# Optimization experiments

Hardware: AMD Instinct MI355X
Metric: run time of the kernel (lower is better)

Reference implementation:

```python
import jax, jax.numpy as jnp
import numpy as np

NODE_DIM = 128
OUT_DIM = 64
N_NODES = 50000
N_EDGES = 800000
NEG_SLOPE = 0.01  # F.leaky_relu default


def setup_inputs() -> dict:
    key = jax.random.key(0)
    k1, k2, k3, k4, k5 = jax.random.split(key, 5)
    h = jax.random.normal(k1, (N_NODES, NODE_DIM), dtype=jnp.float32)
    src = jax.random.randint(k2, (N_EDGES,), 0, N_NODES, dtype=jnp.int32)
    dst = jax.random.randint(k3, (N_EDGES,), 0, N_NODES, dtype=jnp.int32)
    # fc: Linear(node_dim, out_dim, bias=False); attn_fc: Linear(2*out_dim, 1, bias=False)
    W_fc = jax.random.normal(k4, (NODE_DIM, OUT_DIM), dtype=jnp.float32) * (1.0 / np.sqrt(NODE_DIM))
    W_attn = jax.random.normal(k5, (2 * OUT_DIM, 1), dtype=jnp.float32) * (1.0 / np.sqrt(2 * OUT_DIM))
    return {"h": h, "src": src, "dst": dst, "W_fc": W_fc, "W_attn": W_attn}


def reference(h, src, dst, W_fc, W_attn):
    N = h.shape[0]
    D = W_fc.shape[1]
    z = h @ W_fc                                   # [N, D]
    # attn_fc(concat(z_src, z_dst)) == z_src @ Wa[:D] + z_dst @ Wa[D:]
    s_src = (z @ W_attn[:D]).squeeze(-1)            # [N]
    s_dst = (z @ W_attn[D:]).squeeze(-1)            # [N]
    e = jax.nn.leaky_relu(s_src[src] + s_dst[dst], NEG_SLOPE)  # [E]
    # segment softmax over incoming edges per dst node
    m = jax.ops.segment_max(e, dst, num_segments=N)            # [N]
    ex = jnp.exp(e - m[dst])                                   # [E]
    denom = jax.ops.segment_sum(ex, dst, num_segments=N)       # [N]
    alpha = ex / denom[dst]                                    # [E]
    # weighted scatter-sum of src features into dst nodes
    out = jax.ops.segment_sum(alpha[:, None] * z[src], dst, num_segments=N)  # [N, D]
    return out
```

## Files before the change

### kernel.cpp

```cpp
#include <hip/hip_runtime.h>

#define NODE_DIM 128
#define OUT_DIM  64
#define NEG_SLOPE 0.01f
#define EPB    4096
#define BSH    7
#define NPB    128
#define REGCAP 2400

typedef __attribute__((ext_vector_type(8))) short short8;
typedef __attribute__((ext_vector_type(4))) short short4v;
typedef __attribute__((ext_vector_type(4))) float float4e;

__device__ __forceinline__ unsigned short f2bf(float f) {
    unsigned u = __float_as_uint(f);
    unsigned r = (u + 0x7FFFu + ((u >> 16) & 1u)) >> 16;
    return (unsigned short)r;
}
__device__ __forceinline__ float bf2f(unsigned short v) {
    return __uint_as_float((unsigned)v << 16);
}
__device__ __forceinline__ void split_bf(float v, short& hi, short& lo) {
    unsigned short h = f2bf(v);
    float r = v - bf2f(h);
    hi = (short)h;
    lo = (short)f2bf(r);
}

__global__ __launch_bounds__(256) void k_proj_part(
    const float* __restrict__ h, const float* __restrict__ Wf,
    const float* __restrict__ Wa,
    unsigned short* __restrict__ zbf,
    float* __restrict__ s_src, float* __restrict__ s_dst,
    const int* __restrict__ src, const int* __restrict__ dst,
    int* __restrict__ region, int* __restrict__ bcur,
    int N, int E, int nblkP, int NB)
{
    __shared__ union {
        short w[16384];
        unsigned short zt[4][16][68];
        struct { int sd[EPB]; int sv[EPB]; } p;
    } uni;
    __shared__ int cnt[512];
    __shared__ int bb[512];
    __shared__ int rr[512];
    __shared__ int ps[256];

    if (blockIdx.x < (unsigned)nblkP) {
        const int blk = blockIdx.x;
        const int t = threadIdx.x;
        cnt[t] = 0; cnt[t + 256] = 0;
        __syncthreads();
        const int e0 = blk * EPB;
        int nE = E - e0; if (nE > EPB) nE = EPB;

        int db[16], sb[16], rreg[16];
        const int base = e0 + t * 16;
        if (base + 16 <= E) {
            const int4* dp = (const int4*)(dst + base);
            const int4* sp = (const int4*)(src + base);
            #pragma unroll
            for (int q = 0; q < 4; ++q) {
                int4 dv = dp[q], svv = sp[q];
                db[q*4+0]=dv.x; db[q*4+1]=dv.y; db[q*4+2]=dv.z; db[q*4+3]=dv.w;
                sb[q*4+0]=svv.x; sb[q*4+1]=svv.y; sb[q*4+2]=svv.z; sb[q*4+3]=svv.w;
            }
            #pragma unroll
            for (int k = 0; k < 16; ++k)
                rreg[k] = atomicAdd(&cnt[db[k] >> BSH], 1);
        } else {
            #pragma unroll
            for (int k = 0; k < 16; ++k) rreg[k] = -1;
            for (int k = 0; k < 16; ++k) {
                int idx = base + k;
                if (idx < E) {
                    db[k] = dst[idx];
                    sb[k] = src[idx];
                    rreg[k] = atomicAdd(&cnt[db[k] >> BSH], 1);
                }
            }
        }
        __syncthreads();

        int pv = cnt[2 * t] + cnt[2 * t + 1];
        ps[t] = pv;
        __syncthreads();
        #pragma unroll
        for (int off = 1; off < 256; off <<= 1) {
            int u = (t >= off) ? ps[t - off] : 0;
            __syncthreads();
            ps[t] += u;
            __syncthreads();
        }
        int pexc = ps[t] - pv;
        bb[2 * t]     = pexc;
        bb[2 * t + 1] = pexc + cnt[2 * t];
        __syncthreads();

        #pragma unroll
        for (int k = 0; k < 16; ++k) {
            if (rreg[k] >= 0) {
                int pos = bb[db[k] >> BSH] + rreg[k];
                uni.p.sd[pos] = db[k];
                uni.p.sv[pos] = sb[k];
            }
        }
        for (int i = t; i < NB; i += 256) {
            int cb = cnt[i];
            rr[i] = cb ? atomicAdd(bcur + i, cb) : 0;
        }
        __syncthreads();

        for (int j = t; j < nE; j += 256) {
            int d = uni.p.sd[j];
            int b = d >> BSH;
            int gp = rr[b] + (j - bb[b]);
            if (gp < REGCAP)
                region[(size_t)b * REGCAP + gp] = ((d & (NPB - 1)) << 17) | uni.p.sv[j];
        }
        return;
    }

    const int bid  = blockIdx.x - nblkP;
    const int t    = threadIdx.x;
    const int wv   = t >> 6;
    const int lane = t & 63;
    const int m    = lane & 15;
    const int quad = lane >> 4;
    const int row0 = bid * 64 + wv * 16;

    int rowc = row0 + m; if (rowc > N - 1) rowc = N - 1;
    const float* hrow = h + (size_t)rowc * NODE_DIM;
    float4e hreg[8];
    #pragma unroll
    for (int t4 = 0; t4 < 4; ++t4) {
        hreg[t4 * 2]     = *(const float4e*)(hrow + t4 * 32 + quad * 8);
        hreg[t4 * 2 + 1] = *(const float4e*)(hrow + t4 * 32 + quad * 8 + 4);
    }

    {
        short* wh = uni.w;
        short* wl = uni.w + 8192;
        for (int s = t; s < 1024; s += 256) {
            int combo = s >> 6;
            int ln    = s & 63;
            int c = combo >> 2, t4 = combo & 3;
            int col = c * 16 + (ln & 15);
            int kq  = t4 * 32 + (ln >> 4) * 8;
            #pragma unroll
            for (int j = 0; j < 8; ++j) {
                short hi, lo;
                split_bf(Wf[(kq + j) * OUT_DIM + col], hi, lo);
                wh[s * 8 + j] = hi;
                wl[s * 8 + j] = lo;
            }
        }
    }
    __syncthreads();

    short8 Ahi[4], Alo[4];
    #pragma unroll
    for (int t4 = 0; t4 < 4; ++t4) {
        #pragma unroll
        for (int j = 0; j < 4; ++j) {
            short hi, lo;
            split_bf(hreg[t4 * 2][j], hi, lo);
            Ahi[t4][j] = hi; Alo[t4][j] = lo;
            split_bf(hreg[t4 * 2 + 1][j], hi, lo);
            Ahi[t4][4 + j] = hi; Alo[t4][4 + j] = lo;
        }
    }

    float psum[4] = {0.f, 0.f, 0.f, 0.f};
    float pdum[4] = {0.f, 0.f, 0.f, 0.f};
    unsigned short z16[16];

    const short* wh = uni.w;
    const short* wl = uni.w + 8192;
    #pragma unroll
    for (int c = 0; c < 4; ++c) {
        float4e acc = {0.f, 0.f, 0.f, 0.f};
        #pragma unroll
        for (int t4 = 0; t4 < 4; ++t4) {
            int slot = (c * 4 + t4) * 64 + lane;
            short8 bh = *(const short8*)(wh + slot * 8);
            short8 bl = *(const short8*)(wl + slot * 8);
            acc = __builtin_amdgcn_mfma_f32_16x16x32_bf16(Alo[t4], bh, acc, 0, 0, 0);
            acc = __builtin_amdgcn_mfma_f32_16x16x32_bf16(Ahi[t4], bl, acc, 0, 0, 0);
            acc = __builtin_amdgcn_mfma_f32_16x16x32_bf16(Ahi[t4], bh, acc, 0, 0, 0);
        }
        int col = c * 16 + m;
        float was = Wa[col];
        float wad = Wa[OUT_DIM + col];
        #pragma unroll
        for (int r = 0; r < 4; ++r) {
            z16[c * 4 + r] = f2bf(acc[r]);
            psum[r] = fmaf(acc[r], was, psum[r]);
            pdum[r] = fmaf(acc[r], wad, pdum[r]);
        }
    }

    #pragma unroll
    for (int r = 0; r < 4; ++r) {
        #pragma unroll
        for (int off = 1; off < 16; off <<= 1) {
            psum[r] += __shfl_xor(psum[r], off, 64);
            pdum[r] += __shfl_xor(pdum[r], off, 64);
        }
    }
    if (m == 0) {
        #pragma unroll
        for (int r = 0; r < 4; ++r) {
            int nrow = row0 + quad * 4 + r;
            if (nrow < N) { s_src[nrow] = psum[r]; s_dst[nrow] = pdum[r]; }
        }
    }

    __syncthreads();
    {
        unsigned short (*zt)[68] = uni.zt[wv];
        #pragma unroll
        for (int c = 0; c < 4; ++c)
            #pragma unroll
            for (int r = 0; r < 4; ++r)
                zt[quad * 4 + r][c * 16 + m] = z16[c * 4 + r];
        short* zb = (short*)zbf;
        #pragma unroll
        for (int i = 0; i < 2; ++i) {
            int r    = i * 8 + (lane >> 3);
            int colb = (lane & 7) * 8;
            short8 zz = *(const short8*)&zt[r][colb];
            int grow = row0 + r;
            if (grow < N)
                *(short8*)(zb + (size_t)grow * OUT_DIM + colb) = zz;
        }
    }
}

__global__ __launch_bounds__(256) void k_csr(
    const int* __restrict__ region, const int* __restrict__ bcur,
    int* __restrict__ srcG, int* __restrict__ rstartG, int* __restrict__ degG,
    int N)
{
    __shared__ int cntN[NPB], rsN[NPB], curN[NPB], sscan[NPB];
    const int b = blockIdx.x;
    const int t = threadIdx.x;
    int total = bcur[b];
    if (total > REGCAP) total = REGCAP;
    if (t < NPB) cntN[t] = 0;
    __syncthreads();

    const int* reg = region + (size_t)b * REGCAP;
    for (int i = t; i < total; i += 256)
        atomicAdd(&cntN[reg[i] >> 17], 1);
    __syncthreads();

    int vc = 0;
    if (t < NPB) { vc = cntN[t]; sscan[t] = vc; }
    __syncthreads();
    #pragma unroll
    for (int off = 1; off < NPB; off <<= 1) {
        int u = 0;
        if (t < NPB && t >= off) u = sscan[t - off];
        __syncthreads();
        if (t < NPB) sscan[t] += u;
        __syncthreads();
    }
    if (t < NPB) {
        int rs = sscan[t] - vc;
        rsN[t] = rs; curN[t] = rs;
        int node = b * NPB + t;
        if (node < N) {
            rstartG[node] = b * REGCAP + rs;
            degG[node]    = vc;
        }
    }
    __syncthreads();

    int* sg = srcG + (size_t)b * REGCAP;
    for (int i = t; i < total; i += 256) {
        int val = reg[i];
        int pos = atomicAdd(&curN[val >> 17], 1);
        sg[pos] = val & 0x1FFFF;
    }
}

__global__ __launch_bounds__(256) void k_agg(
    const int* __restrict__ srcG, const int* __restrict__ rstartG,
    const int* __restrict__ degG,
    const float* __restrict__ s_src, const float* __restrict__ s_dst,
    const unsigned short* __restrict__ zbf,
    float* __restrict__ out, int N)
{
    const int wv = threadIdx.x >> 6, lane = threadIdx.x & 63;
    const int quad = lane >> 4;
    const int node = blockIdx.x * 16 + wv * 4 + quad;
    if (node >= N) return;
    const int rs = rstartG[node];
    const int dg = degG[node];
    const float sdst = s_dst[node];
    const int cl8 = (lane & 15) * 4;
    const short* zb = (const short*)zbf;

    float a0 = 0.f, a1 = 0.f, a2 = 0.f, a3 = 0.f, den = 0.f;
    int e = 0;
    for (; e + 4 <= dg; e += 4) {
        int s0 = srcG[rs + e], s1 = srcG[rs + e + 1];
        int s2 = srcG[rs + e + 2], s3 = srcG[rs + e + 3];
        float e0 = s_src[s0] + sdst, e1 = s_src[s1] + sdst;
        float e2 = s_src[s2] + sdst, e3 = s_src[s3] + sdst;
        e0 = (e0 > 0.f) ? e0 : e0 * NEG_SLOPE;
        e1 = (e1 > 0.f) ? e1 : e1 * NEG_SLOPE;
        e2 = (e2 > 0.f) ? e2 : e2 * NEG_SLOPE;
        e3 = (e3 > 0.f) ? e3 : e3 * NEG_SLOPE;
        float x0 = __expf(e0), x1 = __expf(e1), x2 = __expf(e2), x3 = __expf(e3);
        short4v z0 = *(const short4v*)(zb + ((size_t)(unsigned)s0 << 6) + cl8);
        short4v z1 = *(const short4v*)(zb + ((size_t)(unsigned)s1 << 6) + cl8);
        short4v z2 = *(const short4v*)(zb + ((size_t)(unsigned)s2 << 6) + cl8);
        short4v z3 = *(const short4v*)(zb + ((size_t)(unsigned)s3 << 6) + cl8);
        den += (x0 + x1) + (x2 + x3);
        a0 = fmaf(x0, bf2f((unsigned short)z0[0]), a0);
        a1 = fmaf(x0, bf2f((unsigned short)z0[1]), a1);
        a2 = fmaf(x0, bf2f((unsigned short)z0[2]), a2);
        a3 = fmaf(x0, bf2f((unsigned short)z0[3]), a3);
        a0 = fmaf(x1, bf2f((unsigned short)z1[0]), a0);
        a1 = fmaf(x1, bf2f((unsigned short)z1[1]), a1);
        a2 = fmaf(x1, bf2f((unsigned short)z1[2]), a2);
        a3 = fmaf(x1, bf2f((unsigned short)z1[3]), a3);
        a0 = fmaf(x2, bf2f((unsigned short)z2[0]), a0);
        a1 = fmaf(x2, bf2f((unsigned short)z2[1]), a1);
        a2 = fmaf(x2, bf2f((unsigned short)z2[2]), a2);
        a3 = fmaf(x2, bf2f((unsigned short)z2[3]), a3);
        a0 = fmaf(x3, bf2f((unsigned short)z3[0]), a0);
        a1 = fmaf(x3, bf2f((unsigned short)z3[1]), a1);
        a2 = fmaf(x3, bf2f((unsigned short)z3[2]), a2);
        a3 = fmaf(x3, bf2f((unsigned short)z3[3]), a3);
    }
    for (; e < dg; ++e) {
        int s0 = srcG[rs + e];
        float e0 = s_src[s0] + sdst;
        e0 = (e0 > 0.f) ? e0 : e0 * NEG_SLOPE;
        float x0 = __expf(e0);
        short4v z0 = *(const short4v*)(zb + ((size_t)(unsigned)s0 << 6) + cl8);
        den += x0;
        a0 = fmaf(x0, bf2f((unsigned short)z0[0]), a0);
        a1 = fmaf(x0, bf2f((unsigned short)z0[1]), a1);
        a2 = fmaf(x0, bf2f((unsigned short)z0[2]), a2);
        a3 = fmaf(x0, bf2f((unsigned short)z0[3]), a3);
    }

    float4e o;
    if (dg > 0) {
        float inv = 1.f / den;
        o[0] = a0 * inv; o[1] = a1 * inv; o[2] = a2 * inv; o[3] = a3 * inv;
    } else {
        o[0] = 0.f; o[1] = 0.f; o[2] = 0.f; o[3] = 0.f;
    }
    *(float4e*)(out + (size_t)node * OUT_DIM + cl8) = o;
}

extern "C" void kernel_launch(void* const* d_in, const int* in_sizes, int n_in,
                              void* d_out, int out_size, void* d_ws, size_t ws_size,
                              hipStream_t stream) {
    const float* h   = (const float*)d_in[0];
    const int*   src = (const int*)d_in[1];
    const int*   dst = (const int*)d_in[2];
    const float* Wf  = (const float*)d_in[3];
    const float* Wa  = (const float*)d_in[4];
    const int N = in_sizes[0] / NODE_DIM;
    const int E = in_sizes[1];
    float* out = (float*)d_out;

    const int PB    = (N + 63) / 64;
    const int nblkP = (E + EPB - 1) / EPB;
    const int NB    = (N + NPB - 1) / NPB;

    char* ws = (char*)d_ws;
    size_t off = 0;
    int* region = (int*)(ws + off);             off += (size_t)NB * REGCAP * sizeof(int);
    int* srcG   = (int*)(ws + off);             off += (size_t)NB * REGCAP * sizeof(int);
    int* bcur   = (int*)(ws + off);             off += (size_t)NB * sizeof(int);
    int* rstartG= (int*)(ws + off);             off += (size_t)N * sizeof(int);
    int* degG   = (int*)(ws + off);             off += (size_t)N * sizeof(int);
    unsigned short* zbf = (unsigned short*)(ws + off); off += (size_t)N * OUT_DIM * sizeof(unsigned short);
    float* s_src = (float*)(ws + off);          off += (size_t)N * sizeof(float);
    float* s_dst = (float*)(ws + off);          off += (size_t)N * sizeof(float);

    hipMemsetAsync(bcur, 0, (size_t)NB * sizeof(int), stream);
    k_proj_part<<<nblkP + PB, 256, 0, stream>>>(h, Wf, Wa, zbf, s_src, s_dst,
                                                src, dst, region, bcur, N, E, nblkP, NB);
    k_csr<<<NB, 256, 0, stream>>>(region, bcur, srcG, rstartG, degG, N);
    k_agg<<<(N + 15) / 16, 256, 0, stream>>>(srcG, rstartG, degG, s_src, s_dst,
                                             zbf, out, N);
}
```

Before: 130.3 us.

## Split aggregation into two column-half launches to shrink per-pass gather footprint

The aggregation kernel now handles only 32 of the 64 output columns per launch, selected by a column offset, and is launched twice. Each lane gathers one 4-byte bf16 pair instead of an 8-byte group. The aim is to halve the z working set touched per pass so more of it stays in cache during random gathers. The cost is that edge indices, attention scores and exponentials are recomputed in both passes, and each gather moves less data per request. An unused shared array in the CSR kernel is also removed.

Result: slower. 142.5 us (+9.3%).

```diff
diff --git a/kernel.cpp b/kernel.cpp
--- a/kernel.cpp
+++ b/kernel.cpp
@@ -9,7 +9,6 @@
 #define REGCAP 2400
 
 typedef __attribute__((ext_vector_type(8))) short short8;
-typedef __attribute__((ext_vector_type(4))) short short4v;
 typedef __attribute__((ext_vector_type(4))) float float4e;
 
 __device__ __forceinline__ unsigned short f2bf(float f) {
@@ -242,7 +241,7 @@
     int* __restrict__ srcG, int* __restrict__ rstartG, int* __restrict__ degG,
     int N)
 {
-    __shared__ int cntN[NPB], rsN[NPB], curN[NPB], sscan[NPB];
+    __shared__ int cntN[NPB], curN[NPB], sscan[NPB];
     const int b = blockIdx.x;
     const int t = threadIdx.x;
     int total = bcur[b];
@@ -268,7 +267,7 @@
     }
     if (t < NPB) {
         int rs = sscan[t] - vc;
-        rsN[t] = rs; curN[t] = rs;
+        curN[t] = rs;
         int node = b * NPB + t;
         if (node < N) {
             rstartG[node] = b * REGCAP + rs;
@@ -290,7 +289,7 @@
     const int* __restrict__ degG,
     const float* __restrict__ s_src, const float* __restrict__ s_dst,
     const unsigned short* __restrict__ zbf,
-    float* __restrict__ out, int N)
+    float* __restrict__ out, int N, int colOff)
 {
     const int wv = threadIdx.x >> 6, lane = threadIdx.x & 63;
     const int quad = lane >> 4;
@@ -299,10 +298,10 @@
     const int rs = rstartG[node];
     const int dg = degG[node];
     const float sdst = s_dst[node];
-    const int cl8 = (lane & 15) * 4;
-    const short* zb = (const short*)zbf;
-
-    float a0 = 0.f, a1 = 0.f, a2 = 0.f, a3 = 0.f, den = 0.f;
+    const int cl = colOff + ((lane & 15) << 1);
+    const unsigned short* zb = zbf + cl;
+
+    float a0 = 0.f, a1 = 0.f, den = 0.f;
     int e = 0;
     for (; e + 4 <= dg; e += 4) {
         int s0 = srcG[rs + e], s1 = srcG[rs + e + 1];
@@ -314,49 +313,39 @@
         e2 = (e2 > 0.f) ? e2 : e2 * NEG_SLOPE;
         e3 = (e3 > 0.f) ? e3 : e3 * NEG_SLOPE;
         float x0 = __expf(e0), x1 = __expf(e1), x2 = __expf(e2), x3 = __expf(e3);
-        short4v z0 = *(const short4v*)(zb + ((size_t)(unsigned)s0 << 6) + cl8);
-        short4v z1 = *(const short4v*)(zb + ((size_t)(unsigned)s1 << 6) + cl8);
-        short4v z2 = *(const short4v*)(zb + ((size_t)(unsigned)s2 << 6) + cl8);
-        short4v z3 = *(const short4v*)(zb + ((size_t)(unsigned)s3 << 6) + cl8);
+        unsigned z0 = *(const unsigned*)(zb + ((size_t)(unsigned)s0 << 6));
+        unsigned z1 = *(const unsigned*)(zb + ((size_t)(unsigned)s1 << 6));
+        unsigned z2 = *(const unsigned*)(zb + ((size_t)(unsigned)s2 << 6));
+        unsigned z3 = *(const unsigned*)(zb + ((size_t)(unsigned)s3 << 6));
         den += (x0 + x1) + (x2 + x3);
-        a0 = fmaf(x0, bf2f((unsigned short)z0[0]), a0);
-        a1 = fmaf(x0, bf2f((unsigned short)z0[1]), a1);
-        a2 = fmaf(x0, bf2f((unsigned short)z0[2]), a2);
-        a3 = fmaf(x0, bf2f((unsigned short)z0[3]), a3);
-        a0 = fmaf(x1, bf2f((unsigned short)z1[0]), a0);
-        a1 = fmaf(x1, bf2f((unsigned short)z1[1]), a1);
-        a2 = fmaf(x1, bf2f((unsigned short)z1[2]), a2);
-        a3 = fmaf(x1, bf2f((unsigned short)z1[3]), a3);
-        a0 = fmaf(x2, bf2f((unsigned short)z2[0]), a0);
-        a1 = fmaf(x2, bf2f((unsigned short)z2[1]), a1);
-        a2 = fmaf(x2, bf2f((unsigned short)z2[2]), a2);
-        a3 = fmaf(x2, bf2f((unsigned short)z2[3]), a3);
-        a0 = fmaf(x3, bf2f((unsigned short)z3[0]), a0);
-        a1 = fmaf(x3, bf2f((unsigned short)z3[1]), a1);
-        a2 = fmaf(x3, bf2f((unsigned short)z3[2]), a2);
-        a3 = fmaf(x3, bf2f((unsigned short)z3[3]), a3);
+        a0 = fmaf(x0, bf2f((unsigned short)(z0 & 0xFFFF)), a0);
+        a1 = fmaf(x0, bf2f((unsigned short)(z0 >> 16)),    a1);
+        a0 = fmaf(x1, bf2f((unsigned short)(z1 & 0xFFFF)), a0);
+        a1 = fmaf(x1, bf2f((unsigned short)(z1 >> 16)),    a1);
+        a0 = fmaf(x2, bf2f((unsigned short)(z2 & 0xFFFF)), a0);
+        a1 = fmaf(x2, bf2f((unsigned short)(z2 >> 16)),    a1);
+        a0 = fmaf(x3, bf2f((unsigned short)(z3 & 0xFFFF)), a0);
+        a1 = fmaf(x3, bf2f((unsigned short)(z3 >> 16)),    a1);
     }
     for (; e < dg; ++e) {
         int s0 = srcG[rs + e];
         float e0 = s_src[s0] + sdst;
         e0 = (e0 > 0.f) ? e0 : e0 * NEG_SLOPE;
         float x0 = __expf(e0);
-        short4v z0 = *(const short4v*)(zb + ((size_t)(unsigned)s0 << 6) + cl8);
+        unsigned z0 = *(const unsigned*)(zb + ((size_t)(unsigned)s0 << 6));
         den += x0;
-        a0 = fmaf(x0, bf2f((unsigned short)z0[0]), a0);
-        a1 = fmaf(x0, bf2f((unsigned short)z0[1]), a1);
-        a2 = fmaf(x0, bf2f((unsigned short)z0[2]), a2);
-        a3 = fmaf(x0, bf2f((unsigned short)z0[3]), a3);
-    }
-
-    float4e o;
+        a0 = fmaf(x0, bf2f((unsigned short)(z0 & 0xFFFF)), a0);
+        a1 = fmaf(x0, bf2f((unsigned short)(z0 >> 16)),    a1);
+    }
+
+    float2 o;
     if (dg > 0) {
         float inv = 1.f / den;
-        o[0] = a0 * inv; o[1] = a1 * inv; o[2] = a2 * inv; o[3] = a3 * inv;
+        o.x = a0 * inv; o.y = a1 * inv;
     } else {
-        o[0] = 0.f; o[1] = 0.f; o[2] = 0.f; o[3] = 0.f;
-    }
-    *(float4e*)(out + (size_t)node * OUT_DIM + cl8) = o;
+        o.x = 0.f; o.y = 0.f;
+    }
+    *(float2*)(out + (size_t)node * OUT_DIM + cl) = o;
 }
 
 extern "C" void kernel_launch(void* const* d_in, const int* in_sizes, int n_in,
@@ -391,5 +380,7 @@
                                                 src, dst, region, bcur, N, E, nblkP, NB);
     k_csr<<<NB, 256, 0, stream>>>(region, bcur, srcG, rstartG, degG, N);
     k_agg<<<(N + 15) / 16, 256, 0, stream>>>(srcG, rstartG, degG, s_src, s_dst,
-                                             zbf, out, N);
-}
+                                             zbf, out, N, 0);
+    k_agg<<<(N + 15) / 16, 256, 0, stream>>>(srcG, rstartG, degG, s_src, s_dst,
+                                             zbf, out, N, 32);
+}
```
